# Kernel optimization log

Measured on AMD Instinct MI355X. Metric: run time of the kernel, lower is better.

The kernel has to match this reference:

```python
import jax, jax.numpy as jnp
import numpy as np

N_NODES = 100000
N_EDGES = 3200000


def gcn_conv(x, edge_index, W, b, num_nodes):
    """PyG GCNConv: x' = D^{-1/2} (A + I) D^{-1/2} (x W) + b (symmetric norm, self-loops)."""
    x = x @ W  # [N, out]
    loop = jnp.arange(num_nodes, dtype=edge_index.dtype)
    src = jnp.concatenate([edge_index[0], loop])
    dst = jnp.concatenate([edge_index[1], loop])
    # degree over destination nodes (incl. self loops)
    deg = jax.ops.segment_sum(jnp.ones_like(dst, dtype=x.dtype), dst, num_segments=num_nodes)
    dinv = jnp.where(deg > 0, jax.lax.rsqrt(deg), 0.0)
    norm = dinv[src] * dinv[dst]  # [E + N]
    msg = x[src] * norm[:, None]  # gather + scale
    out = jax.ops.segment_sum(msg, dst, num_segments=num_nodes)  # scatter-add
    return out + b


def setup_inputs() -> dict:
    key = jax.random.key(0)
    k = jax.random.split(key, 5)
    x = jax.random.normal(k[0], (N_NODES, 256), dtype=jnp.float32)
    edge_index = jax.random.randint(k[1], (2, N_EDGES), 0, N_NODES, dtype=jnp.int64)
    W1 = jax.random.normal(k[2], (256, 16), dtype=jnp.float32) * (1.0 / np.sqrt(256))
    b1 = jnp.zeros((16,), dtype=jnp.float32)
    W2 = jax.random.normal(k[3], (16, 8), dtype=jnp.float32) * (1.0 / np.sqrt(16))
    b2 = jnp.zeros((8,), dtype=jnp.float32)
    return {"x": x, "edge_index": edge_index, "W1": W1, "b1": b1, "W2": W2, "b2": b2}


def reference(x, edge_index, W1, b1, W2, b2):
    n = x.shape[0]
    h = gcn_conv(x, edge_index, W1, b1, n)
    h = jax.nn.relu(h)
    # dropout is identity in eval mode (training=False)
    h = gcn_conv(h, edge_index, W2, b2, n)
    return jax.nn.log_softmax(h, axis=1)
```

## Files before the change

### kernel.cpp

```cpp
#include <hip/hip_runtime.h>

#define NN 100000
#define NE 3200000
#define NB 391
#define CAP 9216
#define PB 16
#define CH_A (256 * PB)
#define BIN_NBLK ((NE + CH_A - 1) / CH_A)
#define GEMM_NBLK (NN / 32)
#define FXS 65536.0f
#define FXI (1.0f / 65536.0f)

typedef _Float16 half4 __attribute__((ext_vector_type(4)));
typedef _Float16 half8 __attribute__((ext_vector_type(8)));

__device__ __forceinline__ float4 f4fma(float s, float4 a, float4 c) {
  c.x = fmaf(s, a.x, c.x); c.y = fmaf(s, a.y, c.y);
  c.z = fmaf(s, a.z, c.z); c.w = fmaf(s, a.w, c.w);
  return c;
}

template<int CTRL>
__device__ __forceinline__ float4 quad_bcast(float4 v) {
  float4 r;
  r.x = __int_as_float(__builtin_amdgcn_update_dpp(__float_as_int(v.x), __float_as_int(v.x), CTRL, 0xF, 0xF, false));
  r.y = __int_as_float(__builtin_amdgcn_update_dpp(__float_as_int(v.y), __float_as_int(v.y), CTRL, 0xF, 0xF, false));
  r.z = __int_as_float(__builtin_amdgcn_update_dpp(__float_as_int(v.z), __float_as_int(v.z), CTRL, 0xF, 0xF, false));
  r.w = __int_as_float(__builtin_amdgcn_update_dpp(__float_as_int(v.w), __float_as_int(v.w), CTRL, 0xF, 0xF, false));
  return r;
}

__global__ __launch_bounds__(256) void k1_kernel(const int* __restrict__ ei,
                                                 int* __restrict__ bucket_cursor,
                                                 int* __restrict__ pairs,
                                                 const float* __restrict__ x,
                                                 const float* __restrict__ W1,
                                                 _Float16* __restrict__ xw1h) {
  int t = threadIdx.x;
  int bid = blockIdx.x;
  if (bid % 5 == 0) {
    int bin_bid = bid / 5;
    __shared__ int  cnt[4][NB];
    __shared__ int  wcur[4][NB];
    __shared__ int  lbase[NB];
    __shared__ int  gbase[NB];
    __shared__ int  sc[512];
    __shared__ int2 stage[CH_A];
    __shared__ int  w64flag;
    int wv = t >> 6;
    for (int k = t; k < 4 * NB; k += 256) (&cnt[0][0])[k] = 0;
    if (t < 64) {
      int o = (t < 32) ? ei[2 * t + 1] : 0;
      unsigned long long bl = __ballot(o != 0);
      if (t == 0) w64flag = (bl == 0ULL) ? 1 : 0;
    }
    __syncthreads();
    bool w64 = (w64flag != 0);
    int base = bin_bid * CH_A;
    int nval = min(CH_A, NE - base);
    int s[PB], d[PB];
    if (w64) {
#pragma unroll
      for (int i = 0; i < 8; ++i) {
        int e0 = base + i * 512 + 2 * t;
        if (e0 < NE) {
          int4 svv = *(const int4*)(ei + 2 * (size_t)e0);
          int4 dvv = *(const int4*)(ei + 2 * (size_t)NE + 2 * (size_t)e0);
          s[2 * i] = svv.x; s[2 * i + 1] = svv.z;
          d[2 * i] = dvv.x; d[2 * i + 1] = dvv.z;
          atomicAdd(&cnt[wv][dvv.x >> 8], 1);
          atomicAdd(&cnt[wv][dvv.z >> 8], 1);
        } else {
          d[2 * i] = -1; d[2 * i + 1] = -1;
        }
      }
    } else {
#pragma unroll
      for (int i = 0; i < PB; ++i) {
        int e = base + i * 256 + t;
        if (e < NE) {
          s[i] = ei[e];
          d[i] = ei[NE + e];
          atomicAdd(&cnt[wv][d[i] >> 8], 1);
        } else {
          d[i] = -1;
        }
      }
    }
    __syncthreads();
    int tA = (t < NB) ? cnt[0][t] + cnt[1][t] + cnt[2][t] + cnt[3][t] : 0;
    int tB = (t + 256 < NB) ? cnt[0][t + 256] + cnt[1][t + 256] + cnt[2][t + 256] + cnt[3][t + 256] : 0;
    sc[t] = tA; sc[t + 256] = tB;
    __syncthreads();
#pragma unroll
    for (int off = 1; off < 512; off <<= 1) {
      int u0 = (t >= off) ? sc[t - off] : 0;
      int u1 = (t + 256 >= off) ? sc[t + 256 - off] : 0;
      __syncthreads();
      sc[t] += u0; sc[t + 256] += u1;
      __syncthreads();
    }
#pragma unroll
    for (int h = 0; h < 2; ++h) {
      int k = t + h * 256;
      if (k < NB) {
        int tot = (h == 0) ? tA : tB;
        int lb = sc[k] - tot;
        lbase[k] = lb;
        gbase[k] = (tot > 0) ? atomicAdd(&bucket_cursor[k], tot) : 0;
        int c0 = cnt[0][k], c1 = cnt[1][k], c2 = cnt[2][k];
        wcur[0][k] = lb;
        wcur[1][k] = lb + c0;
        wcur[2][k] = lb + c0 + c1;
        wcur[3][k] = lb + c0 + c1 + c2;
      }
    }
    __syncthreads();
#pragma unroll
    for (int i = 0; i < PB; ++i) {
      if (d[i] >= 0) {
        int b = d[i] >> 8;
        int slot = atomicAdd(&wcur[wv][b], 1);
        stage[slot] = make_int2(s[i], d[i]);
      }
    }
    __syncthreads();
    for (int k = t; k < nval; k += 256) {
      int2 p = stage[k];
      int b = p.y >> 8;
      pairs[(size_t)b * CAP + gbase[b] + (k - lbase[b])] = p.x | ((p.y & 255) << 24);
    }
  } else {
    const int gid  = bid - bid / 5 - 1;
    const int lane = t & 63;
    const int wv   = t >> 6;
    const int node0 = (gid * 4 + wv) * 8;
    const int cg_ = lane >> 2;
    const int jl = lane & 3;
    float4 w[16];
#pragma unroll
    for (int k = 0; k < 4; ++k)
#pragma unroll
      for (int c = 0; c < 4; ++c)
        w[k * 4 + c] = *(const float4*)(W1 + (cg_ * 16 + k * 4 + c) * 16 + jl * 4);
    float4 xv[8];
#pragma unroll
    for (int i = 0; i < 8; ++i)
      xv[i] = *(const float4*)(x + (size_t)(node0 + i) * 256 + lane * 4);
    float4 acc[8];
#pragma unroll
    for (int i = 0; i < 8; ++i) acc[i] = make_float4(0.f, 0.f, 0.f, 0.f);
#pragma unroll
    for (int i = 0; i < 8; ++i) {
      float4 b = quad_bcast<0x00>(xv[i]);
      acc[i] = f4fma(b.x, w[0], acc[i]);  acc[i] = f4fma(b.y, w[1], acc[i]);
      acc[i] = f4fma(b.z, w[2], acc[i]);  acc[i] = f4fma(b.w, w[3], acc[i]);
    }
#pragma unroll
    for (int i = 0; i < 8; ++i) {
      float4 b = quad_bcast<0x55>(xv[i]);
      acc[i] = f4fma(b.x, w[4], acc[i]);  acc[i] = f4fma(b.y, w[5], acc[i]);
      acc[i] = f4fma(b.z, w[6], acc[i]);  acc[i] = f4fma(b.w, w[7], acc[i]);
    }
#pragma unroll
    for (int i = 0; i < 8; ++i) {
      float4 b = quad_bcast<0xAA>(xv[i]);
      acc[i] = f4fma(b.x, w[8], acc[i]);  acc[i] = f4fma(b.y, w[9], acc[i]);
      acc[i] = f4fma(b.z, w[10], acc[i]); acc[i] = f4fma(b.w, w[11], acc[i]);
    }
#pragma unroll
    for (int i = 0; i < 8; ++i) {
      float4 b = quad_bcast<0xFF>(xv[i]);
      acc[i] = f4fma(b.x, w[12], acc[i]); acc[i] = f4fma(b.y, w[13], acc[i]);
      acc[i] = f4fma(b.z, w[14], acc[i]); acc[i] = f4fma(b.w, w[15], acc[i]);
    }
#pragma unroll
    for (int m = 4; m <= 32; m <<= 1) {
#pragma unroll
      for (int i = 0; i < 8; ++i) {
        acc[i].x += __shfl_xor(acc[i].x, m);
        acc[i].y += __shfl_xor(acc[i].y, m);
        acc[i].z += __shfl_xor(acc[i].z, m);
        acc[i].w += __shfl_xor(acc[i].w, m);
      }
    }
    if (lane < 4) {
#pragma unroll
      for (int i = 0; i < 8; ++i) {
        float4 a = acc[i];
        half4 hv;
        hv[0] = (_Float16)a.x; hv[1] = (_Float16)a.y;
        hv[2] = (_Float16)a.z; hv[3] = (_Float16)a.w;
        *(half4*)(xw1h + (size_t)(node0 + i) * 16 + lane * 4) = hv;
      }
    }
  }
}

__global__ __launch_bounds__(512) void hist_kernel(const int* __restrict__ pairs,
                                                   const int* __restrict__ bucket_cursor,
                                                   float* __restrict__ dinv,
                                                   _Float16* __restrict__ xw1h) {
  __shared__ int hist[2][256];
  __shared__ float dl[256];
  int t = threadIdx.x;
  int b = blockIdx.x;
  int cnt_b = bucket_cursor[b];
  size_t in_base = (size_t)b * CAP;
  if (t < 256) { hist[0][t] = 0; hist[1][t] = 0; }
  __syncthreads();
  int hs = t >> 8;
  for (int i = t; i < cnt_b; i += 1024) {
    int pkA = pairs[in_base + i];
    bool hasB = (i + 512) < cnt_b;
    int pkB = hasB ? pairs[in_base + i + 512] : 0;
    atomicAdd(&hist[hs][((unsigned)pkA) >> 24], 1);
    if (hasB) atomicAdd(&hist[hs][((unsigned)pkB) >> 24], 1);
  }
  __syncthreads();
  if (t < 256) {
    int n = b * 256 + t;
    if (n < NN) {
      float dv = rsqrtf((float)(hist[0][t] + hist[1][t]) + 1.0f);
      dinv[n] = dv;
      dl[t] = dv;
    }
  }
  __syncthreads();
  {
    int n0 = t >> 1, h = t & 1;
    int n = b * 256 + n0;
    if (n < NN) {
      float dv = dl[n0];
      half8* p8 = (half8*)(xw1h + (size_t)n * 16 + h * 8);
      half8 v = *p8;
#pragma unroll
      for (int f = 0; f < 8; ++f) v[f] = (_Float16)((float)v[f] * dv);
      *p8 = v;
    }
  }
}

__global__ __launch_bounds__(1024) void agg1_kernel(const int* __restrict__ pairs,
                                                    const int* __restrict__ bucket_cursor,
                                                    const float* __restrict__ dinv,
                                                    const _Float16* __restrict__ xw1h,
                                                    const float* __restrict__ W2,
                                                    const float* __restrict__ b1,
                                                    _Float16* __restrict__ h1w2h) {
  __shared__ int acc[16][257];
  int t = threadIdx.x;
  int b = blockIdx.x;
  int cnt_b = bucket_cursor[b];
  size_t in_base = (size_t)b * CAP;
  for (int k = t; k < 16 * 257; k += 1024) (&acc[0][0])[k] = 0;
  __syncthreads();
  {
    int hh = t & 1;
    int i0 = t >> 1;
    for (int i = i0; i < cnt_b; i += 1024) {
      int pkA = pairs[in_base + i];
      bool hasB = (i + 512) < cnt_b;
      int pkB = hasB ? pairs[in_base + i + 512] : 0;
      int sA = pkA & 0xFFFFFF, nA = ((unsigned)pkA) >> 24;
      half8 vA = *(const half8*)(xw1h + (size_t)sA * 16 + hh * 8);
      int sB = pkB & 0xFFFFFF, nB = ((unsigned)pkB) >> 24;
      half8 vB;
      if (hasB) vB = *(const half8*)(xw1h + (size_t)sB * 16 + hh * 8);
#pragma unroll
      for (int f = 0; f < 8; ++f)
        atomicAdd(&acc[hh * 8 + f][nA], __float2int_rn((float)vA[f] * FXS));
      if (hasB) {
#pragma unroll
        for (int f = 0; f < 8; ++f)
          atomicAdd(&acc[hh * 8 + f][nB], __float2int_rn((float)vB[f] * FXS));
      }
    }
  }
  __syncthreads();
  int n0 = t >> 2, sub = t & 3;
  int n = b * 256 + n0;
  if (n < NN) {
    float dn = dinv[n];
    half4 sv = *(const half4*)(xw1h + (size_t)n * 16 + sub * 4);
    float4 bv = *(const float4*)(b1 + sub * 4);
    float bb[4] = {bv.x, bv.y, bv.z, bv.w};
    float p[8] = {0.f, 0.f, 0.f, 0.f, 0.f, 0.f, 0.f, 0.f};
    const float4* W2v = (const float4*)W2;
#pragma unroll
    for (int f = 0; f < 4; ++f) {
      int fg = sub * 4 + f;
      float aggv = (float)acc[fg][n0] * FXI;
      float h = fmaxf(fmaf(dn, aggv + (float)sv[f], bb[f]), 0.f);
      float4 wlo = W2v[fg * 2];
      float4 whi = W2v[fg * 2 + 1];
      p[0] = fmaf(h, wlo.x, p[0]); p[1] = fmaf(h, wlo.y, p[1]);
      p[2] = fmaf(h, wlo.z, p[2]); p[3] = fmaf(h, wlo.w, p[3]);
      p[4] = fmaf(h, whi.x, p[4]); p[5] = fmaf(h, whi.y, p[5]);
      p[6] = fmaf(h, whi.z, p[6]); p[7] = fmaf(h, whi.w, p[7]);
    }
#pragma unroll
    for (int m = 1; m <= 2; m <<= 1)
#pragma unroll
      for (int j = 0; j < 8; ++j)
        p[j] += __shfl_xor(p[j], m);
    if (sub == 0) {
      half8 hv;
#pragma unroll
      for (int j = 0; j < 8; ++j) hv[j] = (_Float16)(p[j] * dn);
      *(half8*)(h1w2h + (size_t)n * 8) = hv;
    }
  }
}

__global__ __launch_bounds__(1024) void agg2_kernel(const int* __restrict__ pairs,
                                                    const int* __restrict__ bucket_cursor,
                                                    const float* __restrict__ dinv,
                                                    const _Float16* __restrict__ h1w2h,
                                                    const float* __restrict__ b2,
                                                    float* __restrict__ out) {
  __shared__ int acc[8][257];
  int t = threadIdx.x;
  int b = blockIdx.x;
  int cnt_b = bucket_cursor[b];
  size_t in_base = (size_t)b * CAP;
  for (int k = t; k < 8 * 257; k += 1024) (&acc[0][0])[k] = 0;
  __syncthreads();
  {
    int q = t & 1;
    int i0 = t >> 1;
    for (int i = i0; i < cnt_b; i += 1024) {
      int pkA = pairs[in_base + i];
      bool hasB = (i + 512) < cnt_b;
      int pkB = hasB ? pairs[in_base + i + 512] : 0;
      int sA = pkA & 0xFFFFFF, nA = ((unsigned)pkA) >> 24;
      half4 vA = *(const half4*)(h1w2h + (size_t)sA * 8 + q * 4);
      int sB = pkB & 0xFFFFFF, nB = ((unsigned)pkB) >> 24;
      half4 vB;
      if (hasB) vB = *(const half4*)(h1w2h + (size_t)sB * 8 + q * 4);
#pragma unroll
      for (int f = 0; f < 4; ++f)
        atomicAdd(&acc[q * 4 + f][nA], __float2int_rn((float)vA[f] * FXS));
      if (hasB) {
#pragma unroll
        for (int f = 0; f < 4; ++f)
          atomicAdd(&acc[q * 4 + f][nB], __float2int_rn((float)vB[f] * FXS));
      }
    }
  }
  __syncthreads();
  if (t < 512) {
    int n0 = t >> 1, q = t & 1;
    int n = b * 256 + n0;
    if (n < NN) {
      float dn = dinv[n];
      half4 sv = *(const half4*)(h1w2h + (size_t)n * 8 + q * 4);
      float4 bv = *(const float4*)(b2 + q * 4);
      float v0 = fmaf(dn, (float)acc[q * 4 + 0][n0] * FXI + (float)sv[0], bv.x);
      float v1 = fmaf(dn, (float)acc[q * 4 + 1][n0] * FXI + (float)sv[1], bv.y);
      float v2 = fmaf(dn, (float)acc[q * 4 + 2][n0] * FXI + (float)sv[2], bv.z);
      float v3 = fmaf(dn, (float)acc[q * 4 + 3][n0] * FXI + (float)sv[3], bv.w);
      float mh = fmaxf(fmaxf(v0, v1), fmaxf(v2, v3));
      float m = fmaxf(mh, __shfl_xor(mh, 1));
      float se = expf(v0 - m) + expf(v1 - m) + expf(v2 - m) + expf(v3 - m);
      float st = se + __shfl_xor(se, 1);
      float ls = m + logf(st);
      *(float4*)(out + (size_t)n * 8 + q * 4) = make_float4(v0 - ls, v1 - ls, v2 - ls, v3 - ls);
    }
  }
}

extern "C" void kernel_launch(void* const* d_in, const int* in_sizes, int n_in,
                              void* d_out, int out_size, void* d_ws, size_t ws_size,
                              hipStream_t stream) {
  const float* x  = (const float*)d_in[0];
  const int*   ei = (const int*)d_in[1];
  const float* W1 = (const float*)d_in[2];
  const float* b1 = (const float*)d_in[3];
  const float* W2 = (const float*)d_in[4];
  const float* b2 = (const float*)d_in[5];
  float* out = (float*)d_out;

  float*    dinv          = (float*)d_ws;
  int*      bucket_cursor = (int*)(dinv + NN);
  int*      pairs         = (int*)dinv + 100400;
  _Float16* xw1h  = (_Float16*)(pairs + (size_t)NB * CAP);
  _Float16* h1w2h = xw1h + (size_t)16 * NN;

  hipMemsetAsync(bucket_cursor, 0, (size_t)NB * sizeof(int), stream);
  k1_kernel<<<BIN_NBLK + GEMM_NBLK, 256, 0, stream>>>(ei, bucket_cursor, pairs, x, W1, xw1h);
  hist_kernel<<<NB, 512, 0, stream>>>(pairs, bucket_cursor, dinv, xw1h);
  agg1_kernel<<<NB, 1024, 0, stream>>>(pairs, bucket_cursor, dinv, xw1h, W2, b1, h1w2h);
  agg2_kernel<<<NB, 1024, 0, stream>>>(pairs, bucket_cursor, dinv, h1w2h, b2, out);
}
```

Measured before the change: 267.3 us.

## Fuse hist, agg1, agg2 into one persistent kernel with grid barriers

Merges the three per-bucket kernels into a single launch of NB blocks that are separated by atomic-counter grid barriers. The degree inverse now stays in LDS instead of a global dinv array. This removes two kernel launches and their gaps, plus the global dinv writes and reads. It relies on all 391 blocks of 1024 threads being co-resident; if they are not, the barrier deadlocks. The spin-wait barrier itself also adds some cost.

```diff
diff --git a/kernel.cpp b/kernel.cpp
--- a/kernel.cpp
+++ b/kernel.cpp
@@ -28,6 +28,18 @@
   r.z = __int_as_float(__builtin_amdgcn_update_dpp(__float_as_int(v.z), __float_as_int(v.z), CTRL, 0xF, 0xF, false));
   r.w = __int_as_float(__builtin_amdgcn_update_dpp(__float_as_int(v.w), __float_as_int(v.w), CTRL, 0xF, 0xF, false));
   return r;
+}
+
+__device__ __forceinline__ void gbar(int* bar, int target) {
+  __syncthreads();
+  __threadfence();
+  if (threadIdx.x == 0) {
+    atomicAdd(bar, 1);
+    while (atomicAdd(bar, 0) < target)
+      __builtin_amdgcn_s_sleep(2);
+    __threadfence();
+  }
+  __syncthreads();
 }
 
 __global__ __launch_bounds__(256) void k1_kernel(const int* __restrict__ ei,
@@ -197,41 +209,40 @@
   }
 }
 
-__global__ __launch_bounds__(512) void hist_kernel(const int* __restrict__ pairs,
-                                                   const int* __restrict__ bucket_cursor,
-                                                   float* __restrict__ dinv,
-                                                   _Float16* __restrict__ xw1h) {
-  __shared__ int hist[2][256];
-  __shared__ float dl[256];
+__global__ __launch_bounds__(1024, 8) void k2_kernel(const int* __restrict__ pairs,
+                                                     const int* __restrict__ bucket_cursor,
+                                                     _Float16* __restrict__ xw1h,
+                                                     const float* __restrict__ W2,
+                                                     const float* __restrict__ b1,
+                                                     const float* __restrict__ b2,
+                                                     _Float16* __restrict__ h1w2h,
+                                                     float* __restrict__ out,
+                                                     int* __restrict__ bar) {
+  __shared__ int   acc[16][257];
+  __shared__ int   hist[2][256];
+  __shared__ float dlds[256];
   int t = threadIdx.x;
   int b = blockIdx.x;
   int cnt_b = bucket_cursor[b];
   size_t in_base = (size_t)b * CAP;
+
   if (t < 256) { hist[0][t] = 0; hist[1][t] = 0; }
   __syncthreads();
-  int hs = t >> 8;
-  for (int i = t; i < cnt_b; i += 1024) {
-    int pkA = pairs[in_base + i];
-    bool hasB = (i + 512) < cnt_b;
-    int pkB = hasB ? pairs[in_base + i + 512] : 0;
-    atomicAdd(&hist[hs][((unsigned)pkA) >> 24], 1);
-    if (hasB) atomicAdd(&hist[hs][((unsigned)pkB) >> 24], 1);
-  }
+  int hs = t >> 9;
+  for (int i = t; i < cnt_b; i += 1024)
+    atomicAdd(&hist[hs][((unsigned)pairs[in_base + i]) >> 24], 1);
   __syncthreads();
   if (t < 256) {
     int n = b * 256 + t;
-    if (n < NN) {
-      float dv = rsqrtf((float)(hist[0][t] + hist[1][t]) + 1.0f);
-      dinv[n] = dv;
-      dl[t] = dv;
-    }
-  }
-  __syncthreads();
-  {
+    if (n < NN)
+      dlds[t] = rsqrtf((float)(hist[0][t] + hist[1][t]) + 1.0f);
+  }
+  __syncthreads();
+  if (t < 512) {
     int n0 = t >> 1, h = t & 1;
     int n = b * 256 + n0;
     if (n < NN) {
-      float dv = dl[n0];
+      float dv = dlds[n0];
       half8* p8 = (half8*)(xw1h + (size_t)n * 16 + h * 8);
       half8 v = *p8;
 #pragma unroll
@@ -239,20 +250,8 @@
       *p8 = v;
     }
   }
-}
-
-__global__ __launch_bounds__(1024) void agg1_kernel(const int* __restrict__ pairs,
-                                                    const int* __restrict__ bucket_cursor,
-                                                    const float* __restrict__ dinv,
-                                                    const _Float16* __restrict__ xw1h,
-                                                    const float* __restrict__ W2,
-                                                    const float* __restrict__ b1,
-                                                    _Float16* __restrict__ h1w2h) {
-  __shared__ int acc[16][257];
-  int t = threadIdx.x;
-  int b = blockIdx.x;
-  int cnt_b = bucket_cursor[b];
-  size_t in_base = (size_t)b * CAP;
+  gbar(bar, NB);
+
   for (int k = t; k < 16 * 257; k += 1024) (&acc[0][0])[k] = 0;
   __syncthreads();
   {
@@ -278,52 +277,43 @@
     }
   }
   __syncthreads();
-  int n0 = t >> 2, sub = t & 3;
-  int n = b * 256 + n0;
-  if (n < NN) {
-    float dn = dinv[n];
-    half4 sv = *(const half4*)(xw1h + (size_t)n * 16 + sub * 4);
-    float4 bv = *(const float4*)(b1 + sub * 4);
-    float bb[4] = {bv.x, bv.y, bv.z, bv.w};
-    float p[8] = {0.f, 0.f, 0.f, 0.f, 0.f, 0.f, 0.f, 0.f};
-    const float4* W2v = (const float4*)W2;
-#pragma unroll
-    for (int f = 0; f < 4; ++f) {
-      int fg = sub * 4 + f;
-      float aggv = (float)acc[fg][n0] * FXI;
-      float h = fmaxf(fmaf(dn, aggv + (float)sv[f], bb[f]), 0.f);
-      float4 wlo = W2v[fg * 2];
-      float4 whi = W2v[fg * 2 + 1];
-      p[0] = fmaf(h, wlo.x, p[0]); p[1] = fmaf(h, wlo.y, p[1]);
-      p[2] = fmaf(h, wlo.z, p[2]); p[3] = fmaf(h, wlo.w, p[3]);
-      p[4] = fmaf(h, whi.x, p[4]); p[5] = fmaf(h, whi.y, p[5]);
-      p[6] = fmaf(h, whi.z, p[6]); p[7] = fmaf(h, whi.w, p[7]);
-    }
-#pragma unroll
-    for (int m = 1; m <= 2; m <<= 1)
-#pragma unroll
-      for (int j = 0; j < 8; ++j)
-        p[j] += __shfl_xor(p[j], m);
-    if (sub == 0) {
-      half8 hv;
-#pragma unroll
-      for (int j = 0; j < 8; ++j) hv[j] = (_Float16)(p[j] * dn);
-      *(half8*)(h1w2h + (size_t)n * 8) = hv;
-    }
-  }
-}
-
-__global__ __launch_bounds__(1024) void agg2_kernel(const int* __restrict__ pairs,
-                                                    const int* __restrict__ bucket_cursor,
-                                                    const float* __restrict__ dinv,
-                                                    const _Float16* __restrict__ h1w2h,
-                                                    const float* __restrict__ b2,
-                                                    float* __restrict__ out) {
-  __shared__ int acc[8][257];
-  int t = threadIdx.x;
-  int b = blockIdx.x;
-  int cnt_b = bucket_cursor[b];
-  size_t in_base = (size_t)b * CAP;
+  {
+    int n0 = t >> 2, sub = t & 3;
+    int n = b * 256 + n0;
+    if (n < NN) {
+      float dn = dlds[n0];
+      half4 sv = *(const half4*)(xw1h + (size_t)n * 16 + sub * 4);
+      float4 bv = *(const float4*)(b1 + sub * 4);
+      float bb[4] = {bv.x, bv.y, bv.z, bv.w};
+      float p[8] = {0.f, 0.f, 0.f, 0.f, 0.f, 0.f, 0.f, 0.f};
+      const float4* W2v = (const float4*)W2;
+#pragma unroll
+      for (int f = 0; f < 4; ++f) {
+        int fg = sub * 4 + f;
+        float aggv = (float)acc[fg][n0] * FXI;
+        float h = fmaxf(fmaf(dn, aggv + (float)sv[f], bb[f]), 0.f);
+        float4 wlo = W2v[fg * 2];
+        float4 whi = W2v[fg * 2 + 1];
+        p[0] = fmaf(h, wlo.x, p[0]); p[1] = fmaf(h, wlo.y, p[1]);
+        p[2] = fmaf(h, wlo.z, p[2]); p[3] = fmaf(h, wlo.w, p[3]);
+        p[4] = fmaf(h, whi.x, p[4]); p[5] = fmaf(h, whi.y, p[5]);
+        p[6] = fmaf(h, whi.z, p[6]); p[7] = fmaf(h, whi.w, p[7]);
+      }
+#pragma unroll
+      for (int m = 1; m <= 2; m <<= 1)
+#pragma unroll
+        for (int j = 0; j < 8; ++j)
+          p[j] += __shfl_xor(p[j], m);
+      if (sub == 0) {
+        half8 hv;
+#pragma unroll
+        for (int j = 0; j < 8; ++j) hv[j] = (_Float16)(p[j] * dn);
+        *(half8*)(h1w2h + (size_t)n * 8) = hv;
+      }
+    }
+  }
+  gbar(bar, 2 * NB);
+
   for (int k = t; k < 8 * 257; k += 1024) (&acc[0][0])[k] = 0;
   __syncthreads();
   {
@@ -353,7 +343,7 @@
     int n0 = t >> 1, q = t & 1;
     int n = b * 256 + n0;
     if (n < NN) {
-      float dn = dinv[n];
+      float dn = dlds[n0];
       half4 sv = *(const half4*)(h1w2h + (size_t)n * 8 + q * 4);
       float4 bv = *(const float4*)(b2 + q * 4);
       float v0 = fmaf(dn, (float)acc[q * 4 + 0][n0] * FXI + (float)sv[0], bv.x);
@@ -381,15 +371,14 @@
   const float* b2 = (const float*)d_in[5];
   float* out = (float*)d_out;
 
-  float*    dinv          = (float*)d_ws;
-  int*      bucket_cursor = (int*)(dinv + NN);
-  int*      pairs         = (int*)dinv + 100400;
+  int*      bucket_cursor = (int*)d_ws;
+  int*      bar           = bucket_cursor + NB;
+  int*      pairs         = bucket_cursor + 400;
   _Float16* xw1h  = (_Float16*)(pairs + (size_t)NB * CAP);
   _Float16* h1w2h = xw1h + (size_t)16 * NN;
 
-  hipMemsetAsync(bucket_cursor, 0, (size_t)NB * sizeof(int), stream);
+  hipMemsetAsync(bucket_cursor, 0, (size_t)(NB + 1) * sizeof(int), stream);
   k1_kernel<<<BIN_NBLK + GEMM_NBLK, 256, 0, stream>>>(ei, bucket_cursor, pairs, x, W1, xw1h);
-  hist_kernel<<<NB, 512, 0, stream>>>(pairs, bucket_cursor, dinv, xw1h);
-  agg1_kernel<<<NB, 1024, 0, stream>>>(pairs, bucket_cursor, dinv, xw1h, W2, b1, h1w2h);
-  agg2_kernel<<<NB, 1024, 0, stream>>>(pairs, bucket_cursor, dinv, h1w2h, b2, out);
-}
+  k2_kernel<<<NB, 1024, 0, stream>>>(pairs, bucket_cursor, xw1h, W2, b1, b2,
+                                     h1w2h, out, bar);
+}
```

Measured after the change: 521.0 us. 1.95x slower.
